# Optimization experiments

Measured on AMD Instinct MI355X. Metric: run time of the kernel, lower is better.

## Reference

```python
import jax, jax.numpy as jnp
import numpy as np

D_SCALED = 8  # adaptive pool output spatial size


def setup_inputs() -> dict:
    key = jax.random.key(0)
    ks = jax.random.split(key, 5)
    b, t, c, h, w = 8, 16, 64, 56, 56
    d_t = 16
    d_in = D_SCALED * D_SCALED  # 64
    d_out = d_t * 2             # 32
    return {
        "x": jax.random.normal(ks[0], (b, t, c, h, w), dtype=jnp.float32),
        "Wq": jax.random.normal(ks[1], (d_in, d_out), dtype=jnp.float32) * 0.001,
        "bq": jax.random.normal(ks[2], (d_out,), dtype=jnp.float32) * 0.001,
        "Wk": jax.random.normal(ks[3], (d_in, d_out), dtype=jnp.float32) * 0.001,
        "bk": jax.random.normal(ks[4], (d_out,), dtype=jnp.float32) * 0.001,
    }


def reference(x, Wq, bq, Wk, bk):
    b, t, c, h, w = x.shape
    ds = D_SCALED
    # shift_x: [b, c, t, h, w]
    shift = jnp.transpose(x, (0, 2, 1, 3, 4))
    # AdaptiveAvgPool3d((None, ds, ds)): h,w divide evenly -> reshape-mean
    pooled = shift.reshape(b, c, t, ds, h // ds, ds, w // ds).mean(axis=(4, 6))
    flat = pooled.reshape(b * c, t, ds * ds)          # [bc, t, ds*ds]
    q = flat @ Wq + bq                                # [bc, t, 2*d_t]
    k = flat @ Wk + bk                                # [bc, t, 2*d_t]
    att = jnp.einsum('ntd,nsd->nts', q, k) / np.sqrt(t).astype(jnp.float32)
    att = jax.nn.softmax(att, axis=-1)                # [bc, t, t]
    v = shift.reshape(b * c, t, h * w)                # [bc, t, h*w]
    out = jnp.einsum('nts,nsv->ntv', att, v)          # [bc, t, h*w]
    out = out.reshape(b, c, t, h, w)
    return jnp.transpose(out, (0, 2, 1, 3, 4))        # [b, t, c, h, w]
```

## Files before the change

### kernel.cpp

```cpp
#include <hip/hip_runtime.h>
#include <math.h>

#define B  8
#define T  16
#define C  64
#define H  56
#define W  56
#define HW (H*W)
#define HW4 (HW/4)
#define DS 8
#define DIN (DS*DS)
#define DOUT 32
#define BC (B*C)

typedef float vfloat4 __attribute__((ext_vector_type(4)));


__global__ __launch_bounds__(256) void pool_kernel(const float* __restrict__ x,
                                                   float* __restrict__ pooled_g) {
    __shared__ float xs[HW];
    __shared__ float part[256];
    const int n = blockIdx.x;
    const int t = blockIdx.y;
    const int tid = threadIdx.x;
    const int b = n >> 6;
    const int c = n & 63;

    const float4* x4 = (const float4*)x;
    float4* xs4 = (float4*)xs;
    const size_t base = ((size_t)(b * T + t) * C + c) * HW4;

    for (int i = tid; i < HW4; i += 256) xs4[i] = x4[base + i];
    __syncthreads();

    {
        const int wi = tid & 63;
        const int q  = tid >> 6;
        const int ri = wi >> 3;
        const int rj = wi & 7;
        const int r0 = 2 * q;
        const int nrows = (q < 3) ? 2 : 1;
        float s = 0.f;
        for (int dr = 0; dr < nrows; ++dr) {
            const int row = 7 * ri + r0 + dr;
            const int col0 = 7 * rj;
            #pragma unroll
            for (int dj = 0; dj < 7; ++dj) s += xs[row * W + col0 + dj];
        }
        part[q * 64 + wi] = s;
    }
    __syncthreads();

    if (tid < 64) {
        const float v = part[tid] + part[tid + 64] + part[tid + 128] + part[tid + 192];
        pooled_g[((size_t)n * T + t) * DIN + tid] = v * (1.0f / 49.0f);
    }
}

__global__ __launch_bounds__(256) void att_kernel(const float* __restrict__ pooled_g,
                                                  const float* __restrict__ Wq,
                                                  const float* __restrict__ bq,
                                                  const float* __restrict__ Wk,
                                                  const float* __restrict__ bk,
                                                  float* __restrict__ att_g) {
    __shared__ float pooled_s[T * DIN];
    __shared__ float qs[T * 33];
    __shared__ float ks[T * 33];
    __shared__ float att_s[T * T];

    const int n = blockIdx.x;
    const int tid = threadIdx.x;

    for (int e = tid; e < T * DIN; e += 256) pooled_s[e] = pooled_g[(size_t)n * (T * DIN) + e];
    __syncthreads();

    for (int e = tid; e < T * DOUT; e += 256) {
        const int t = e >> 5;
        const int d = e & 31;
        float sq = bq[d];
        float sk = bk[d];
        #pragma unroll 8
        for (int kk = 0; kk < DIN; ++kk) {
            const float f = pooled_s[t * DIN + kk];
            sq = fmaf(f, Wq[kk * DOUT + d], sq);
            sk = fmaf(f, Wk[kk * DOUT + d], sk);
        }
        qs[t * 33 + d] = sq;
        ks[t * 33 + d] = sk;
    }
    __syncthreads();

    {
        const int tt = tid >> 4;
        const int ss = tid & 15;
        float s = 0.f;
        #pragma unroll
        for (int d = 0; d < DOUT; ++d) s = fmaf(qs[tt * 33 + d], ks[ss * 33 + d], s);
        att_s[tid] = s * 0.25f;
    }
    __syncthreads();

    if (tid < T) {
        const int r = tid;
        float m = -INFINITY;
        #pragma unroll
        for (int s = 0; s < T; ++s) m = fmaxf(m, att_s[r * T + s]);
        float e[T];
        float sum = 0.f;
        #pragma unroll
        for (int s = 0; s < T; ++s) { e[s] = __expf(att_s[r * T + s] - m); sum += e[s]; }
        const float inv = 1.0f / sum;
        #pragma unroll
        for (int s = 0; s < T; ++s) att_g[(size_t)n * (T * T) + r * T + s] = e[s] * inv;
    }
}

__global__ __launch_bounds__(128) void apply_kernel(const float* __restrict__ x,
                                                    const float* __restrict__ att_g,
                                                    float* __restrict__ out) {
    __shared__ float att_tr[T * T];
    const int n = blockIdx.x;
    const int chunk = blockIdx.y;
    const int tid = threadIdx.x;
    const int b = n >> 6;
    const int c = n & 63;

    #pragma unroll
    for (int e = tid; e < T * T; e += 128) {
        const int t = e >> 4;
        const int s = e & 15;
        att_tr[s * T + t] = att_g[(size_t)n * (T * T) + e];
    }
    __syncthreads();

    if (tid < 112) {
        const float4* x4 = (const float4*)x;
        float4* o4 = (float4*)out;
        const float4* att4 = (const float4*)att_tr;
        const size_t xbase = ((size_t)(b * T) * C + c) * HW4;
        const size_t tstride = (size_t)C * HW4;
        const int p4 = chunk * 112 + tid;

        float4 acc[16];
        #pragma unroll
        for (int t = 0; t < 16; ++t) acc[t] = make_float4(0.f, 0.f, 0.f, 0.f);

        #pragma unroll 4
        for (int s = 0; s < T; ++s) {
            const float4 xv = x4[xbase + (size_t)s * tstride + p4];
            #pragma unroll
            for (int q = 0; q < 4; ++q) {
                const float4 a = att4[s * 4 + q];
                acc[q*4+0].x = fmaf(a.x, xv.x, acc[q*4+0].x);
                acc[q*4+0].y = fmaf(a.x, xv.y, acc[q*4+0].y);
                acc[q*4+0].z = fmaf(a.x, xv.z, acc[q*4+0].z);
                acc[q*4+0].w = fmaf(a.x, xv.w, acc[q*4+0].w);
                acc[q*4+1].x = fmaf(a.y, xv.x, acc[q*4+1].x);
                acc[q*4+1].y = fmaf(a.y, xv.y, acc[q*4+1].y);
                acc[q*4+1].z = fmaf(a.y, xv.z, acc[q*4+1].z);
                acc[q*4+1].w = fmaf(a.y, xv.w, acc[q*4+1].w);
                acc[q*4+2].x = fmaf(a.z, xv.x, acc[q*4+2].x);
                acc[q*4+2].y = fmaf(a.z, xv.y, acc[q*4+2].y);
                acc[q*4+2].z = fmaf(a.z, xv.z, acc[q*4+2].z);
                acc[q*4+2].w = fmaf(a.z, xv.w, acc[q*4+2].w);
                acc[q*4+3].x = fmaf(a.w, xv.x, acc[q*4+3].x);
                acc[q*4+3].y = fmaf(a.w, xv.y, acc[q*4+3].y);
                acc[q*4+3].z = fmaf(a.w, xv.z, acc[q*4+3].z);
                acc[q*4+3].w = fmaf(a.w, xv.w, acc[q*4+3].w);
            }
        }

        #pragma unroll
        for (int t = 0; t < 16; ++t) {
            vfloat4* dst = (vfloat4*)&o4[xbase + (size_t)t * tstride + p4];
            vfloat4 v; v.x = acc[t].x; v.y = acc[t].y; v.z = acc[t].z; v.w = acc[t].w;
            __builtin_nontemporal_store(v, dst);
        }
    }
}

extern "C" void kernel_launch(void* const* d_in, const int* in_sizes, int n_in,
                              void* d_out, int out_size, void* d_ws, size_t ws_size,
                              hipStream_t stream) {
    const float* x  = (const float*)d_in[0];
    const float* Wq = (const float*)d_in[1];
    const float* bq = (const float*)d_in[2];
    const float* Wk = (const float*)d_in[3];
    const float* bk = (const float*)d_in[4];
    float* out = (float*)d_out;

    float* pooled_g = out;
    float* att_g = (float*)d_ws;

    pool_kernel<<<dim3(BC, T), dim3(256), 0, stream>>>(x, pooled_g);
    att_kernel<<<dim3(BC), dim3(256), 0, stream>>>(pooled_g, Wq, bq, Wk, bk, att_g);
    apply_kernel<<<dim3(BC, 7), dim3(128), 0, stream>>>(x, att_g, out);
}
```

Baseline: 211.6 us.

## Fuse attention computation into apply kernel, recomputing per chunk block

Merges the attention (q/k projection, scores, softmax) kernel into the apply kernel so each of the 7 spatial-chunk blocks per channel recomputes its 16x16 attention matrix in shared memory. This removes one kernel launch and the global round trip of the attention matrix. The pooled buffer moves to workspace since the output is now written concurrently. It trades this for redundant per-block compute and extra latency before streaming x.

```diff
diff --git a/kernel.cpp b/kernel.cpp
--- a/kernel.cpp
+++ b/kernel.cpp
@@ -57,24 +57,36 @@
     }
 }
 
-__global__ __launch_bounds__(256) void att_kernel(const float* __restrict__ pooled_g,
-                                                  const float* __restrict__ Wq,
-                                                  const float* __restrict__ bq,
-                                                  const float* __restrict__ Wk,
-                                                  const float* __restrict__ bk,
-                                                  float* __restrict__ att_g) {
+__global__ __launch_bounds__(128) void att_apply_kernel(const float* __restrict__ x,
+                                                        const float* __restrict__ pooled_g,
+                                                        const float* __restrict__ Wq,
+                                                        const float* __restrict__ bq,
+                                                        const float* __restrict__ Wk,
+                                                        const float* __restrict__ bk,
+                                                        float* __restrict__ out) {
     __shared__ float pooled_s[T * DIN];
     __shared__ float qs[T * 33];
-    __shared__ float ks[T * 33];
+    __shared__ float ksh[T * 33];
     __shared__ float att_s[T * T];
+    __shared__ float att_tr[T * T];
 
     const int n = blockIdx.x;
+    const int chunk = blockIdx.y;
     const int tid = threadIdx.x;
+    const int b = n >> 6;
+    const int c = n & 63;
 
-    for (int e = tid; e < T * DIN; e += 256) pooled_s[e] = pooled_g[(size_t)n * (T * DIN) + e];
+    {
+        const float4* pg4 = (const float4*)(pooled_g + (size_t)n * (T * DIN));
+        float4* ps4 = (float4*)pooled_s;
+        ps4[tid] = pg4[tid];
+        ps4[tid + 128] = pg4[tid + 128];
+    }
     __syncthreads();
 
-    for (int e = tid; e < T * DOUT; e += 256) {
+    #pragma unroll
+    for (int j = 0; j < 4; ++j) {
+        const int e = tid + 128 * j;
         const int t = e >> 5;
         const int d = e & 31;
         float sq = bq[d];
@@ -86,17 +98,19 @@
             sk = fmaf(f, Wk[kk * DOUT + d], sk);
         }
         qs[t * 33 + d] = sq;
-        ks[t * 33 + d] = sk;
+        ksh[t * 33 + d] = sk;
     }
     __syncthreads();
 
-    {
-        const int tt = tid >> 4;
-        const int ss = tid & 15;
+    #pragma unroll
+    for (int j = 0; j < 2; ++j) {
+        const int e = tid + 128 * j;
+        const int tt = e >> 4;
+        const int ss = e & 15;
         float s = 0.f;
         #pragma unroll
-        for (int d = 0; d < DOUT; ++d) s = fmaf(qs[tt * 33 + d], ks[ss * 33 + d], s);
-        att_s[tid] = s * 0.25f;
+        for (int d = 0; d < DOUT; ++d) s = fmaf(qs[tt * 33 + d], ksh[ss * 33 + d], s);
+        att_s[e] = s * 0.25f;
     }
     __syncthreads();
 
@@ -111,25 +125,7 @@
         for (int s = 0; s < T; ++s) { e[s] = __expf(att_s[r * T + s] - m); sum += e[s]; }
         const float inv = 1.0f / sum;
         #pragma unroll
-        for (int s = 0; s < T; ++s) att_g[(size_t)n * (T * T) + r * T + s] = e[s] * inv;
-    }
-}
-
-__global__ __launch_bounds__(128) void apply_kernel(const float* __restrict__ x,
-                                                    const float* __restrict__ att_g,
-                                                    float* __restrict__ out) {
-    __shared__ float att_tr[T * T];
-    const int n = blockIdx.x;
-    const int chunk = blockIdx.y;
-    const int tid = threadIdx.x;
-    const int b = n >> 6;
-    const int c = n & 63;
-
-    #pragma unroll
-    for (int e = tid; e < T * T; e += 128) {
-        const int t = e >> 4;
-        const int s = e & 15;
-        att_tr[s * T + t] = att_g[(size_t)n * (T * T) + e];
+        for (int s = 0; s < T; ++s) att_tr[s * T + r] = e[s] * inv;
     }
     __syncthreads();
 
@@ -189,10 +185,8 @@
     const float* bk = (const float*)d_in[4];
     float* out = (float*)d_out;
 
-    float* pooled_g = out;
-    float* att_g = (float*)d_ws;
+    float* pooled_g = (float*)d_ws;
 
     pool_kernel<<<dim3(BC, T), dim3(256), 0, stream>>>(x, pooled_g);
-    att_kernel<<<dim3(BC), dim3(256), 0, stream>>>(pooled_g, Wq, bq, Wk, bk, att_g);
-    apply_kernel<<<dim3(BC, 7), dim3(128), 0, stream>>>(x, att_g, out);
+    att_apply_kernel<<<dim3(BC, 7), dim3(128), 0, stream>>>(x, pooled_g, Wq, bq, Wk, bk, out);
 }
```

Result: slower. 229.7 us (+8.6%).

## Flatten apply kernel over all columns with 256-thread blocks and pre-transposed attention

Applied to the files above, without the earlier changes.

The apply kernel now uses a flat 1D grid where each 256-thread block covers 256 consecutive float4 columns, which can span two (b,c) slices. Both attention matrices are loaded into LDS and selected per thread, so no threads sit idle as the 16 out of 128 did before. The attention kernel now writes the softmax output already transposed, which removes the in-kernel transpose. Nontemporal stores are replaced with plain stores, which may change cache behaviour on the large output write.

```diff
diff --git a/kernel.cpp b/kernel.cpp
--- a/kernel.cpp
+++ b/kernel.cpp
@@ -12,6 +12,7 @@
 #define DIN (DS*DS)
 #define DOUT 32
 #define BC (B*C)
+#define NCOL (BC*HW4)
 
 typedef float vfloat4 __attribute__((ext_vector_type(4)));
 
@@ -111,71 +112,68 @@
         for (int s = 0; s < T; ++s) { e[s] = __expf(att_s[r * T + s] - m); sum += e[s]; }
         const float inv = 1.0f / sum;
         #pragma unroll
-        for (int s = 0; s < T; ++s) att_g[(size_t)n * (T * T) + r * T + s] = e[s] * inv;
+        for (int s = 0; s < T; ++s) att_g[(size_t)n * (T * T) + s * T + r] = e[s] * inv;
     }
 }
 
-__global__ __launch_bounds__(128) void apply_kernel(const float* __restrict__ x,
+__global__ __launch_bounds__(256) void apply_kernel(const float* __restrict__ x,
                                                     const float* __restrict__ att_g,
                                                     float* __restrict__ out) {
-    __shared__ float att_tr[T * T];
-    const int n = blockIdx.x;
-    const int chunk = blockIdx.y;
+    __shared__ float att_lds[2 * 256];
     const int tid = threadIdx.x;
-    const int b = n >> 6;
-    const int c = n & 63;
+    const int blk0 = blockIdx.x << 8;
+    const int n0 = blk0 / HW4;
+    const int n1 = (blk0 + 255) / HW4;
+
+    att_lds[tid]       = att_g[(size_t)n0 * 256 + tid];
+    att_lds[256 + tid] = att_g[(size_t)n1 * 256 + tid];
+    __syncthreads();
+
+    const int Wf  = blk0 + tid;
+    const int n   = Wf / HW4;
+    const int col = Wf - n * HW4;
+    const int b   = n >> 6;
+    const int c   = n & 63;
+    const float* att_p = att_lds + ((n != n0) ? 256 : 0);
+    const float4* att4 = (const float4*)att_p;
+
+    const float4* x4 = (const float4*)x;
+    float4* o4 = (float4*)out;
+    const size_t xbase = ((size_t)b * T * C + c) * HW4 + col;
+    const size_t tstride = (size_t)C * HW4;
+
+    float4 acc[16];
+    #pragma unroll
+    for (int t = 0; t < 16; ++t) acc[t] = make_float4(0.f, 0.f, 0.f, 0.f);
+
+    #pragma unroll 4
+    for (int s = 0; s < T; ++s) {
+        const float4 xv = x4[xbase + (size_t)s * tstride];
+        #pragma unroll
+        for (int q = 0; q < 4; ++q) {
+            const float4 a = att4[s * 4 + q];
+            acc[q*4+0].x = fmaf(a.x, xv.x, acc[q*4+0].x);
+            acc[q*4+0].y = fmaf(a.x, xv.y, acc[q*4+0].y);
+            acc[q*4+0].z = fmaf(a.x, xv.z, acc[q*4+0].z);
+            acc[q*4+0].w = fmaf(a.x, xv.w, acc[q*4+0].w);
+            acc[q*4+1].x = fmaf(a.y, xv.x, acc[q*4+1].x);
+            acc[q*4+1].y = fmaf(a.y, xv.y, acc[q*4+1].y);
+            acc[q*4+1].z = fmaf(a.y, xv.z, acc[q*4+1].z);
+            acc[q*4+1].w = fmaf(a.y, xv.w, acc[q*4+1].w);
+            acc[q*4+2].x = fmaf(a.z, xv.x, acc[q*4+2].x);
+            acc[q*4+2].y = fmaf(a.z, xv.y, acc[q*4+2].y);
+            acc[q*4+2].z = fmaf(a.z, xv.z, acc[q*4+2].z);
+            acc[q*4+2].w = fmaf(a.z, xv.w, acc[q*4+2].w);
+            acc[q*4+3].x = fmaf(a.w, xv.x, acc[q*4+3].x);
+            acc[q*4+3].y = fmaf(a.w, xv.y, acc[q*4+3].y);
+            acc[q*4+3].z = fmaf(a.w, xv.z, acc[q*4+3].z);
+            acc[q*4+3].w = fmaf(a.w, xv.w, acc[q*4+3].w);
+        }
+    }
 
     #pragma unroll
-    for (int e = tid; e < T * T; e += 128) {
-        const int t = e >> 4;
-        const int s = e & 15;
-        att_tr[s * T + t] = att_g[(size_t)n * (T * T) + e];
-    }
-    __syncthreads();
-
-    if (tid < 112) {
-        const float4* x4 = (const float4*)x;
-        float4* o4 = (float4*)out;
-        const float4* att4 = (const float4*)att_tr;
-        const size_t xbase = ((size_t)(b * T) * C + c) * HW4;
-        const size_t tstride = (size_t)C * HW4;
-        const int p4 = chunk * 112 + tid;
-
-        float4 acc[16];
-        #pragma unroll
-        for (int t = 0; t < 16; ++t) acc[t] = make_float4(0.f, 0.f, 0.f, 0.f);
-
-        #pragma unroll 4
-        for (int s = 0; s < T; ++s) {
-            const float4 xv = x4[xbase + (size_t)s * tstride + p4];
-            #pragma unroll
-            for (int q = 0; q < 4; ++q) {
-                const float4 a = att4[s * 4 + q];
-                acc[q*4+0].x = fmaf(a.x, xv.x, acc[q*4+0].x);
-                acc[q*4+0].y = fmaf(a.x, xv.y, acc[q*4+0].y);
-                acc[q*4+0].z = fmaf(a.x, xv.z, acc[q*4+0].z);
-                acc[q*4+0].w = fmaf(a.x, xv.w, acc[q*4+0].w);
-                acc[q*4+1].x = fmaf(a.y, xv.x, acc[q*4+1].x);
-                acc[q*4+1].y = fmaf(a.y, xv.y, acc[q*4+1].y);
-                acc[q*4+1].z = fmaf(a.y, xv.z, acc[q*4+1].z);
-                acc[q*4+1].w = fmaf(a.y, xv.w, acc[q*4+1].w);
-                acc[q*4+2].x = fmaf(a.z, xv.x, acc[q*4+2].x);
-                acc[q*4+2].y = fmaf(a.z, xv.y, acc[q*4+2].y);
-                acc[q*4+2].z = fmaf(a.z, xv.z, acc[q*4+2].z);
-                acc[q*4+2].w = fmaf(a.z, xv.w, acc[q*4+2].w);
-                acc[q*4+3].x = fmaf(a.w, xv.x, acc[q*4+3].x);
-                acc[q*4+3].y = fmaf(a.w, xv.y, acc[q*4+3].y);
-                acc[q*4+3].z = fmaf(a.w, xv.z, acc[q*4+3].z);
-                acc[q*4+3].w = fmaf(a.w, xv.w, acc[q*4+3].w);
-            }
-        }
-
-        #pragma unroll
-        for (int t = 0; t < 16; ++t) {
-            vfloat4* dst = (vfloat4*)&o4[xbase + (size_t)t * tstride + p4];
-            vfloat4 v; v.x = acc[t].x; v.y = acc[t].y; v.z = acc[t].z; v.w = acc[t].w;
-            __builtin_nontemporal_store(v, dst);
-        }
+    for (int t = 0; t < 16; ++t) {
+        o4[xbase + (size_t)t * tstride] = acc[t];
     }
 }
 
@@ -194,5 +192,5 @@
 
     pool_kernel<<<dim3(BC, T), dim3(256), 0, stream>>>(x, pooled_g);
     att_kernel<<<dim3(BC), dim3(256), 0, stream>>>(pooled_g, Wq, bq, Wk, bk, att_g);
-    apply_kernel<<<dim3(BC, 7), dim3(128), 0, stream>>>(x, att_g, out);
+    apply_kernel<<<dim3(NCOL / 256), dim3(256), 0, stream>>>(x, att_g, out);
 }
```

Result: no change. 211.2 us (-0.2%).
